# Performance work log

Hardware: AMD Instinct MI355X
Metric: run time of the kernel (lower is better)

## Reference

```python
import jax, jax.numpy as jnp
import numpy as np
import math

B, Q, CQ = 2, 2048, 512
H, D = 8, 64  # no_heads, c_hidden

def setup_inputs() -> dict:
    key = jax.random.key(0)
    ks = jax.random.split(key, 8)
    s = 0.02
    return {
        "q_x": jax.random.normal(ks[0], (B, Q, CQ), jnp.float32),
        "kv_x": jax.random.normal(ks[1], (B, Q, CQ), jnp.float32),
        "bias": jax.random.normal(ks[2], (B, 1, Q, Q), jnp.float32),
        "w_qkv": jax.random.normal(ks[3], (3 * H * D, CQ), jnp.float32) * s,
        "w_o": jax.random.normal(ks[4], (CQ, H * D), jnp.float32) * s,
        "b_o": jnp.zeros((CQ,), jnp.float32),
        "w_g": jax.random.normal(ks[5], (H * D, CQ), jnp.float32) * s,
        "b_g": jnp.zeros((H * D,), jnp.float32),
    }

def reference(q_x, kv_x, bias, w_qkv, w_o, b_o, w_g, b_g):
    # Fused QKV projection from q_x (kv_x is unused by the original module's _prep_qkv)
    qkv = jnp.einsum('bqc,ec->bqe', q_x, w_qkv)  # [B,Q,3*H*D]
    q, k, v = jnp.split(qkv, 3, axis=-1)
    q = q.reshape(B, Q, H, D) / math.sqrt(D)
    k = k.reshape(B, Q, H, D)
    v = v.reshape(B, Q, H, D)
    # scores + additive pairwise bias, softmax over keys
    scores = jnp.einsum('bqhd,bkhd->bhqk', q, k) + bias  # [B,H,Q,K]
    attn = jax.nn.softmax(scores, axis=-1)
    o = jnp.einsum('bhqk,bkhd->bqhd', attn, v)  # [B,Q,H,D]
    # sigmoid gating
    g = jax.nn.sigmoid(jnp.einsum('bqc,ec->bqe', q_x, w_g) + b_g).reshape(B, Q, H, D)
    o = o * g
    # output projection
    o = o.reshape(B, Q, H * D)
    return jnp.einsum('bqe,ce->bqc', o, w_o) + b_o
```

## Files before the change

### kernel.cpp

```cpp
#include <hip/hip_runtime.h>
#include <math.h>

#define B_  2
#define Q_  2048
#define CQ_ 512
#define H_  8
#define D_  64
#define M_  (B_*Q_)
#define L2E 1.44269504088896f

typedef __bf16 bf16;
typedef __bf16 bf16x4 __attribute__((ext_vector_type(4)));
typedef __bf16 bf16x8 __attribute__((ext_vector_type(8)));
typedef float  f32x4  __attribute__((ext_vector_type(4)));
typedef float  f32x16 __attribute__((ext_vector_type(16)));
typedef unsigned int u32x2 __attribute__((ext_vector_type(2)));

__device__ __forceinline__ void gl_lds16(const bf16* g, bf16* l) {
    __builtin_amdgcn_global_load_lds(
        (const __attribute__((address_space(1))) unsigned int*)g,
        (__attribute__((address_space(3))) unsigned int*)l, 16, 0, 0);
}

__device__ __forceinline__ unsigned int cvtpk_bf16(float lo, float hi) {
    unsigned int r;
    asm("v_cvt_pk_bf16_f32 %0, %1, %2" : "=v"(r) : "v"(lo), "v"(hi));
    return r;
}

#define S0 (4096*512)
#define S1 (1536*512)
#define S2 (512*512)
#define S3 (512*512)
__global__ __launch_bounds__(256)
void convert_kernel(const float* __restrict__ qx, const float* __restrict__ wqkv,
                    const float* __restrict__ wg, const float* __restrict__ wo,
                    bf16* __restrict__ qxb, bf16* __restrict__ wcat, bf16* __restrict__ wob)
{
    const long long t = (long long)blockIdx.x * 256 + threadIdx.x;
    const long long e = t * 8;
    const float* src; bf16* dst;
    if (e < S0)                { src = qx + e;                  dst = qxb + e; }
    else if (e < S0 + S1)      { src = wqkv + (e - S0);         dst = wcat + (e - S0); }
    else if (e < S0 + S1 + S2) { src = wg + (e - S0 - S1);      dst = wcat + S1 + (e - S0 - S1); }
    else                       { src = wo + (e - S0 - S1 - S2); dst = wob + (e - S0 - S1 - S2); }
    const float4 a = *(const float4*)(src);
    const float4 b = *(const float4*)(src + 4);
    bf16x8 v;
    v[0] = (bf16)a.x; v[1] = (bf16)a.y; v[2] = (bf16)a.z; v[3] = (bf16)a.w;
    v[4] = (bf16)b.x; v[5] = (bf16)b.y; v[6] = (bf16)b.z; v[7] = (bf16)b.w;
    *(bf16x8*)dst = v;
}

__global__ __launch_bounds__(256)
void bias_rearrange(const float* __restrict__ bias, float* __restrict__ bT)
{
    __shared__ float lds[2048];
    const int x = blockIdx.x;
    const int b = x >> 11, q32 = (x >> 5) & 63, kt = x & 31;
    const int t = threadIdx.x;
    const int qo = t >> 3, kc = (t & 7) * 8;
    const float* src = bias + ((size_t)b * Q_ + q32 * 32 + qo) * Q_ + kt * 64 + kc;
    const float4 a = *(const float4*)src;
    const float4 c = *(const float4*)(src + 4);
    const float v[8] = {a.x, a.y, a.z, a.w, c.x, c.y, c.z, c.w};
    #pragma unroll
    for (int j2 = 0; j2 < 8; ++j2) {
        const int ko = kc + j2;
        const int i  = (ko >> 5) * 4 + ((ko >> 3) & 3);
        const int b5 = (ko >> 2) & 1;
        const int j  = ko & 3;
        lds[i * 256 + b5 * 128 + qo * 4 + j] = v[j2];
    }
    __syncthreads();
    float* outp = bT + ((size_t)(b * 64 + q32) * 32 + kt) * 2048 + t * 8;
    *(float4*)(outp)     = *(const float4*)(lds + t * 8);
    *(float4*)(outp + 4) = *(const float4*)(lds + t * 8 + 4);
}

template<int BM, int BN, int EPI>
__global__ __launch_bounds__(256)
void gemm_bf16(const bf16* __restrict__ A, const bf16* __restrict__ W,
               const float* __restrict__ bvec, float* __restrict__ fout,
               bf16* __restrict__ qb, bf16* __restrict__ kb, bf16* __restrict__ vb,
               bf16* __restrict__ gb)
{
    constexpr int MI = BM / 32, NJ = BN / 32;
    __shared__ __align__(16) bf16 As[BM * 32];
    __shared__ __align__(16) bf16 Bs[BN * 32];

    const int t = threadIdx.x;
    const int w = t >> 6, lane = t & 63;
    const int l15 = lane & 15, quad = lane >> 4;
    const int wm = w & 1, wn = w >> 1;
    const int bm = blockIdx.x * BM;
    const int bn = blockIdx.y * BN;
    const bool swapped = (EPI == 1) || ((bn >> 9) != 2);

    f32x4 acc[MI][NJ] = {};

    const int rr = t >> 2;
    const int cc = (t & 3) * 8;

    for (int k0 = 0; k0 < 512; k0 += 32) {
        #pragma unroll
        for (int i = 0; i < BM / 64; ++i)
            gl_lds16(A + (size_t)(bm + i * 64 + rr) * 512 + k0 + cc,
                     As + (i * 64 + w * 16) * 32);
        #pragma unroll
        for (int i = 0; i < BN / 64; ++i)
            gl_lds16(W + (size_t)(bn + i * 64 + rr) * 512 + k0 + cc,
                     Bs + (i * 64 + w * 16) * 32);
        __asm__ volatile("s_waitcnt vmcnt(0)" ::: "memory");
        __syncthreads();

        bf16x8 af[MI], bfr[NJ];
        #pragma unroll
        for (int i = 0; i < MI; ++i)
            af[i] = *(const bf16x8*)(As + (wm * (BM / 2) + i * 16 + l15) * 32 + quad * 8);
        #pragma unroll
        for (int j = 0; j < NJ; ++j)
            bfr[j] = *(const bf16x8*)(Bs + (wn * (BN / 2) + j * 16 + l15) * 32 + quad * 8);
        if (swapped) {
            #pragma unroll
            for (int i = 0; i < MI; ++i)
                #pragma unroll
                for (int j = 0; j < NJ; ++j)
                    acc[i][j] = __builtin_amdgcn_mfma_f32_16x16x32_bf16(bfr[j], af[i], acc[i][j], 0, 0, 0);
        } else {
            #pragma unroll
            for (int i = 0; i < MI; ++i)
                #pragma unroll
                for (int j = 0; j < NJ; ++j)
                    acc[i][j] = __builtin_amdgcn_mfma_f32_16x16x32_bf16(af[i], bfr[j], acc[i][j], 0, 0, 0);
        }
        __syncthreads();
    }

    if (swapped) {
        #pragma unroll
        for (int i = 0; i < MI; ++i) {
            const int m = bm + wm * (BM / 2) + i * 16 + l15;
            const int b = m >> 11, qq = m & 2047;
            #pragma unroll
            for (int j = 0; j < NJ; ++j) {
                const int n0 = bn + wn * (BN / 2) + j * 16 + quad * 4;
                const f32x4 cv = acc[i][j];
                if constexpr (EPI == 1) {
                    float4 st;
                    st.x = cv[0] + bvec[n0 + 0];
                    st.y = cv[1] + bvec[n0 + 1];
                    st.z = cv[2] + bvec[n0 + 2];
                    st.w = cv[3] + bvec[n0 + 3];
                    *(float4*)(fout + (size_t)m * 512 + n0) = st;
                } else {
                    const int part = n0 >> 9;
                    if (part == 0) {
                        const int h = (n0 >> 6) & 7, d0 = n0 & 63;
                        bf16x4 q4;
                        #pragma unroll
                        for (int r = 0; r < 4; ++r) q4[r] = (bf16)(cv[r] * (0.125f * L2E));
                        *(bf16x4*)(qb + (size_t)(b * H_ + h) * (Q_ * D_) + (size_t)qq * 64 + d0) = q4;
                    } else if (part == 1) {
                        const int h = (n0 >> 6) & 7, d0 = n0 & 63;
                        const size_t off = (size_t)(b * H_ + h) * (Q_ * D_)
                            + (qq >> 6) * 4096 + ((qq >> 5) & 1) * 2048
                            + (d0 >> 4) * 512 + ((d0 >> 3) & 1) * 256
                            + (qq & 31) * 8 + (d0 & 7);
                        bf16x4 k4;
                        #pragma unroll
                        for (int r = 0; r < 4; ++r) k4[r] = (bf16)cv[r];
                        *(bf16x4*)(kb + off) = k4;
                    } else {
                        const int gcol = n0 & 511;
                        const float4 bv4 = *(const float4*)(bvec + gcol);
                        bf16x4 g4;
                        g4[0] = (bf16)(1.f / (1.f + __expf(-(cv[0] + bv4.x))));
                        g4[1] = (bf16)(1.f / (1.f + __expf(-(cv[1] + bv4.y))));
                        g4[2] = (bf16)(1.f / (1.f + __expf(-(cv[2] + bv4.z))));
                        g4[3] = (bf16)(1.f / (1.f + __expf(-(cv[3] + bv4.w))));
                        *(bf16x4*)(gb + (size_t)m * 512 + gcol) = g4;
                    }
                }
            }
        }
    } else {
        #pragma unroll
        for (int i = 0; i < MI; ++i) {
            const int m0 = bm + wm * (BM / 2) + i * 16 + quad * 4;
            const int b = m0 >> 11, qq0 = m0 & 2047;
            #pragma unroll
            for (int j = 0; j < NJ; ++j) {
                const int n = bn + wn * (BN / 2) + j * 16 + l15;
                const int h = (n >> 6) & 7, d = n & 63;
                const size_t off = (size_t)(b * H_ + h) * (Q_ * D_)
                    + (qq0 >> 6) * 4096 + (d >> 5) * 2048
                    + ((qq0 & 63) >> 4) * 512 + ((qq0 >> 3) & 1) * 256
                    + (d & 31) * 8 + (qq0 & 7);
                bf16x4 v4;
                #pragma unroll
                for (int r = 0; r < 4; ++r) v4[r] = (bf16)acc[i][j][r];
                *(bf16x4*)(vb + off) = v4;
            }
        }
    }
}

__global__ __launch_bounds__(256, 3)
void attn_part(const bf16* __restrict__ qb, const bf16* __restrict__ kf,
               const bf16* __restrict__ vf, const float* __restrict__ bT,
               bf16* __restrict__ po, float2* __restrict__ ml)
{
    __shared__ __align__(16) bf16 Ks[2][4096];
    __shared__ __align__(16) bf16 Vs[2][4096];

    const int tid  = threadIdx.x;
    const int wv   = tid >> 6, lane = tid & 63;
    const int l31  = lane & 31, b5 = lane >> 5;
    const int x    = blockIdx.x;
    const int bh   = ((x & 7) << 1) | (x >> 3);
    const int b    = bh >> 3;
    const int qg   = blockIdx.y * 128 + wv * 32 + l31;
    const int ks   = blockIdx.z;
    const int t0   = ks * 11;
    const int nt   = (ks < 2) ? 11 : 10;

    const bf16* qp = qb + ((size_t)bh * Q_ + qg) * D_;
    bf16x8 bq[4];
    #pragma unroll
    for (int c = 0; c < 4; ++c)
        bq[c] = *(const bf16x8*)(qp + c * 16 + b5 * 8);

    f32x16 acc[2] = {};
    float m_run = -INFINITY, l_run = 0.f;

    const bf16*  kfb  = kf + (size_t)bh * (Q_ * D_) + (size_t)t0 * 4096;
    const bf16*  vfb  = vf + (size_t)bh * (Q_ * D_) + (size_t)t0 * 4096;
    const int q32 = blockIdx.y * 4 + wv;
    const float* brow = bT + (((size_t)b * 64 + q32) * 32 + t0) * 2048;

    f32x4 nb[8];

    #pragma unroll
    for (int p = 0; p < 2; ++p) {
        gl_lds16(kfb + (wv * 2 + p) * 512 + lane * 8, Ks[0] + (wv * 2 + p) * 512);
        gl_lds16(vfb + (wv * 2 + p) * 512 + lane * 8, Vs[0] + (wv * 2 + p) * 512);
    }
    #pragma unroll
    for (int i = 0; i < 8; ++i)
        nb[i] = *(const f32x4*)(brow + i * 256 + lane * 4);
    __asm__ volatile("s_waitcnt vmcnt(0)" ::: "memory");
    __syncthreads();

    int cur = 0;
    #pragma unroll 1
    for (int t = 0; t < nt; ++t) {
        if (t < nt - 1) {
            const size_t off = (size_t)(t + 1) * 4096;
            #pragma unroll
            for (int p = 0; p < 2; ++p) {
                gl_lds16(kfb + off + (wv * 2 + p) * 512 + lane * 8,
                         Ks[cur ^ 1] + (wv * 2 + p) * 512);
                gl_lds16(vfb + off + (wv * 2 + p) * 512 + lane * 8,
                         Vs[cur ^ 1] + (wv * 2 + p) * 512);
            }
        }
        __asm__ volatile("" ::: "memory");

        f32x16 sv[2];
        #pragma unroll
        for (int kg = 0; kg < 2; ++kg)
            #pragma unroll
            for (int r = 0; r < 16; ++r)
                sv[kg][r] = nb[kg * 4 + (r >> 2)][r & 3] * L2E;

        if (t < nt - 1) {
            const float* bnx = brow + (size_t)(t + 1) * 2048;
            #pragma unroll
            for (int i = 0; i < 8; ++i)
                nb[i] = *(const f32x4*)(bnx + i * 256 + lane * 4);
        }
        __asm__ volatile("" ::: "memory");

        const bf16* Kc = Ks[cur];
        __builtin_amdgcn_s_setprio(1);
        #pragma unroll
        for (int kg = 0; kg < 2; ++kg)
            #pragma unroll
            for (int c = 0; c < 4; ++c) {
                const bf16x8 ak = *(const bf16x8*)(Kc + kg * 2048 + c * 512 + lane * 8);
                sv[kg] = __builtin_amdgcn_mfma_f32_32x32x16_bf16(ak, bq[c], sv[kg], 0, 0, 0);
            }
        __builtin_amdgcn_s_setprio(0);

        float mx[16];
        #pragma unroll
        for (int r = 0; r < 16; ++r) mx[r] = fmaxf(sv[0][r], sv[1][r]);
        #pragma unroll
        for (int r = 0; r < 8; ++r) mx[r] = fmaxf(mx[r], mx[r + 8]);
        #pragma unroll
        for (int r = 0; r < 4; ++r) mx[r] = fmaxf(mx[r], mx[r + 4]);
        float tmax = fmaxf(fmaxf(mx[0], mx[1]), fmaxf(mx[2], mx[3]));
        tmax = fmaxf(tmax, __shfl_xor(tmax, 32, 64));

        const float mn = fmaxf(m_run, tmax);
        const float alpha = __builtin_amdgcn_exp2f(m_run - mn);
        m_run = mn;

        #pragma unroll
        for (int kg = 0; kg < 2; ++kg)
            #pragma unroll
            for (int r = 0; r < 16; ++r)
                sv[kg][r] = __builtin_amdgcn_exp2f(sv[kg][r] - mn);

        float sm[16];
        #pragma unroll
        for (int r = 0; r < 16; ++r) sm[r] = sv[0][r] + sv[1][r];
        #pragma unroll
        for (int r = 0; r < 8; ++r) sm[r] += sm[r + 8];
        #pragma unroll
        for (int r = 0; r < 4; ++r) sm[r] += sm[r + 4];
        float rsum = (sm[0] + sm[1]) + (sm[2] + sm[3]);
        rsum += __shfl_xor(rsum, 32, 64);
        l_run = l_run * alpha + rsum;
        acc[0] *= alpha;
        acc[1] *= alpha;

        bf16x8 bp[4];
        #pragma unroll
        for (int kg = 0; kg < 2; ++kg)
            #pragma unroll
            for (int h = 0; h < 2; ++h) {
                const unsigned int u  = cvtpk_bf16(sv[kg][8 * h + 0], sv[kg][8 * h + 1]);
                const unsigned int u2 = cvtpk_bf16(sv[kg][8 * h + 2], sv[kg][8 * h + 3]);
                const unsigned int vv = cvtpk_bf16(sv[kg][8 * h + 4], sv[kg][8 * h + 5]);
                const unsigned int v2 = cvtpk_bf16(sv[kg][8 * h + 6], sv[kg][8 * h + 7]);
                const u32x2 s1 = __builtin_amdgcn_permlane32_swap(u,  vv, false, false);
                const u32x2 s2 = __builtin_amdgcn_permlane32_swap(u2, v2, false, false);
                union { unsigned int w[4]; bf16x8 v8; } pkw;
                pkw.w[0] = s1[0]; pkw.w[1] = s2[0]; pkw.w[2] = s1[1]; pkw.w[3] = s2[1];
                bp[kg * 2 + h] = pkw.v8;
            }

        const bf16* Vc = Vs[cur];
        __builtin_amdgcn_s_setprio(1);
        #pragma unroll
        for (int c4 = 0; c4 < 4; ++c4) {
            #pragma unroll
            for (int dg = 0; dg < 2; ++dg) {
                const bf16x8 av = *(const bf16x8*)(Vc + dg * 2048 + c4 * 512 + lane * 8);
                acc[dg] = __builtin_amdgcn_mfma_f32_32x32x16_bf16(av, bp[c4], acc[dg], 0, 0, 0);
            }
        }
        __builtin_amdgcn_s_setprio(0);

        __asm__ volatile("s_waitcnt vmcnt(8)" ::: "memory");
        __syncthreads();
        cur ^= 1;
    }

    const float inv = 1.f / l_run;
    const size_t pbase = ((size_t)(ks * 16 + bh) * Q_ + qg) * 64;
    #pragma unroll
    for (int dg = 0; dg < 2; ++dg)
        #pragma unroll
        for (int gi = 0; gi < 4; ++gi) {
            const int d0 = dg * 32 + gi * 8 + b5 * 4;
            bf16x4 ov;
            #pragma unroll
            for (int r = 0; r < 4; ++r)
                ov[r] = (bf16)(acc[dg][gi * 4 + r] * inv);
            *(bf16x4*)(po + pbase + d0) = ov;
        }
    if (b5 == 0)
        ml[(size_t)(ks * 16 + bh) * Q_ + qg] = make_float2(m_run, l_run);
}

__global__ __launch_bounds__(256)
void merge_kernel(const bf16* __restrict__ po, const float2* __restrict__ ml,
                  const bf16* __restrict__ g, bf16* __restrict__ og)
{
    const int gid = blockIdx.x * 256 + threadIdx.x;
    const int row = gid >> 3;
    const int d8  = (gid & 7) * 8;
    const int bh  = row >> 11, qg = row & 2047;
    const int b   = bh >> 3, h = bh & 7;

    float2 m4[3];
    #pragma unroll
    for (int s = 0; s < 3; ++s) m4[s] = ml[(size_t)s * (16 * Q_) + row];
    const float M = fmaxf(fmaxf(m4[0].x, m4[1].x), m4[2].x);
    float w[3], tot = 0.f;
    #pragma unroll
    for (int s = 0; s < 3; ++s) {
        w[s] = m4[s].y * __builtin_amdgcn_exp2f(m4[s].x - M);
        tot += w[s];
    }
    const float inv = 1.f / tot;
    #pragma unroll
    for (int s = 0; s < 3; ++s) w[s] *= inv;

    bf16x8 o[3];
    #pragma unroll
    for (int s = 0; s < 3; ++s)
        o[s] = *(const bf16x8*)(po + (size_t)s * (16 * Q_ * 64) + (size_t)row * 64 + d8);

    const size_t obase = ((size_t)(b * Q_ + qg)) * 512 + h * 64 + d8;
    const bf16x8 gv = *(const bf16x8*)(g + obase);
    bf16x8 ov;
    #pragma unroll
    for (int r = 0; r < 8; ++r) {
        float acc = 0.f;
        #pragma unroll
        for (int s = 0; s < 3; ++s) acc += (float)o[s][r] * w[s];
        ov[r] = (bf16)(acc * (float)gv[r]);
    }
    *(bf16x8*)(og + obase) = ov;
}

extern "C" void kernel_launch(void* const* d_in, const int* in_sizes, int n_in,
                              void* d_out, int out_size, void* d_ws, size_t ws_size,
                              hipStream_t stream)
{
    const float* q_x   = (const float*)d_in[0];
    const float* bias  = (const float*)d_in[2];
    const float* w_qkv = (const float*)d_in[3];
    const float* w_o   = (const float*)d_in[4];
    const float* b_o   = (const float*)d_in[5];
    const float* w_g   = (const float*)d_in[6];
    const float* b_g   = (const float*)d_in[7];
    float* out = (float*)d_out;

    char* ws = (char*)d_ws;
    bf16*   qxb  = (bf16*)(ws);
    bf16*   wcat = (bf16*)(ws + (4u  << 20));
    bf16*   po   = (bf16*)(ws);
    bf16*   qb   = (bf16*)(ws + (16u << 20));
    bf16*   kb   = (bf16*)(ws + (20u << 20));
    bf16*   vb   = (bf16*)(ws + (24u << 20));
    bf16*   gb   = (bf16*)(ws + (28u << 20));
    bf16*   ogb  = (bf16*)(ws + (32u << 20));
    bf16*   wob  = (bf16*)(ws + (36u << 20));
    float2* ml   = (float2*)(ws + (36u << 20) + (1u << 19));
    float*  bT   = (float*)(ws + (38u << 20));

    convert_kernel<<<(S0 + S1 + S2 + S3) / (256 * 8), 256, 0, stream>>>(
        q_x, w_qkv, w_g, w_o, qxb, wcat, wob);
    bias_rearrange<<<B_ * 64 * 32, 256, 0, stream>>>(bias, bT);
    gemm_bf16<128, 128, 0><<<dim3(32, 16), 256, 0, stream>>>(
        qxb, wcat, b_g, nullptr, qb, kb, vb, gb);
    attn_part<<<dim3(B_ * H_, Q_ / 128, 3), 256, 0, stream>>>(qb, kb, vb, bT, po, ml);
    merge_kernel<<<(16 * Q_ * 8) / 256, 256, 0, stream>>>(po, ml, gb, ogb);
    gemm_bf16<64, 128, 1><<<dim3(64, 4), 256, 0, stream>>>(
        ogb, wob, b_o, out, nullptr, nullptr, nullptr, nullptr);
}
```

Before: 178.8 us.

## Fuse prep kernels, fold split-K merge into output GEMM, lazy softmax rescale

Merges the bf16 conversion and bias rearrangement into one launch and pre-multiplies the bias by log2(e) there, removing a per-tile multiply in attention. The attention loop now skips the running-max update and accumulator rescale when the new tile max stays within 8 (log2 units) of the current max, across the whole wavefront. The split-K merge and gating are moved into the A-tile load of a dedicated output GEMM, which removes a kernel launch and the intermediate gated-output buffer round trip. In exchange, each of the 4 column blocks of the output GEMM recomputes the merge, and the lazy rescale relies on exp2 of values up to 2^8 staying in range.

```diff
diff --git a/kernel.cpp b/kernel.cpp
--- a/kernel.cpp
+++ b/kernel.cpp
@@ -32,56 +32,57 @@
 #define S1 (1536*512)
 #define S2 (512*512)
 #define S3 (512*512)
+#define NCV ((S0 + S1 + S2 + S3) / (256 * 8))
 __global__ __launch_bounds__(256)
 void convert_kernel(const float* __restrict__ qx, const float* __restrict__ wqkv,
                     const float* __restrict__ wg, const float* __restrict__ wo,
-                    bf16* __restrict__ qxb, bf16* __restrict__ wcat, bf16* __restrict__ wob)
-{
-    const long long t = (long long)blockIdx.x * 256 + threadIdx.x;
-    const long long e = t * 8;
-    const float* src; bf16* dst;
-    if (e < S0)                { src = qx + e;                  dst = qxb + e; }
-    else if (e < S0 + S1)      { src = wqkv + (e - S0);         dst = wcat + (e - S0); }
-    else if (e < S0 + S1 + S2) { src = wg + (e - S0 - S1);      dst = wcat + S1 + (e - S0 - S1); }
-    else                       { src = wo + (e - S0 - S1 - S2); dst = wob + (e - S0 - S1 - S2); }
-    const float4 a = *(const float4*)(src);
-    const float4 b = *(const float4*)(src + 4);
-    bf16x8 v;
-    v[0] = (bf16)a.x; v[1] = (bf16)a.y; v[2] = (bf16)a.z; v[3] = (bf16)a.w;
-    v[4] = (bf16)b.x; v[5] = (bf16)b.y; v[6] = (bf16)b.z; v[7] = (bf16)b.w;
-    *(bf16x8*)dst = v;
-}
-
-__global__ __launch_bounds__(256)
-void bias_rearrange(const float* __restrict__ bias, float* __restrict__ bT)
+                    const float* __restrict__ bias,
+                    bf16* __restrict__ qxb, bf16* __restrict__ wcat,
+                    bf16* __restrict__ wob, float* __restrict__ bT)
 {
     __shared__ float lds[2048];
-    const int x = blockIdx.x;
-    const int b = x >> 11, q32 = (x >> 5) & 63, kt = x & 31;
-    const int t = threadIdx.x;
-    const int qo = t >> 3, kc = (t & 7) * 8;
-    const float* src = bias + ((size_t)b * Q_ + q32 * 32 + qo) * Q_ + kt * 64 + kc;
-    const float4 a = *(const float4*)src;
-    const float4 c = *(const float4*)(src + 4);
-    const float v[8] = {a.x, a.y, a.z, a.w, c.x, c.y, c.z, c.w};
-    #pragma unroll
-    for (int j2 = 0; j2 < 8; ++j2) {
-        const int ko = kc + j2;
-        const int i  = (ko >> 5) * 4 + ((ko >> 3) & 3);
-        const int b5 = (ko >> 2) & 1;
-        const int j  = ko & 3;
-        lds[i * 256 + b5 * 128 + qo * 4 + j] = v[j2];
-    }
-    __syncthreads();
-    float* outp = bT + ((size_t)(b * 64 + q32) * 32 + kt) * 2048 + t * 8;
-    *(float4*)(outp)     = *(const float4*)(lds + t * 8);
-    *(float4*)(outp + 4) = *(const float4*)(lds + t * 8 + 4);
-}
-
-template<int BM, int BN, int EPI>
+    const int bx = blockIdx.x;
+    const int t  = threadIdx.x;
+    if (bx < NCV) {
+        const long long e = ((long long)bx * 256 + t) * 8;
+        const float* src; bf16* dst;
+        if (e < S0)                { src = qx + e;                  dst = qxb + e; }
+        else if (e < S0 + S1)      { src = wqkv + (e - S0);         dst = wcat + (e - S0); }
+        else if (e < S0 + S1 + S2) { src = wg + (e - S0 - S1);      dst = wcat + S1 + (e - S0 - S1); }
+        else                       { src = wo + (e - S0 - S1 - S2); dst = wob + (e - S0 - S1 - S2); }
+        const float4 a = *(const float4*)(src);
+        const float4 b = *(const float4*)(src + 4);
+        bf16x8 v;
+        v[0] = (bf16)a.x; v[1] = (bf16)a.y; v[2] = (bf16)a.z; v[3] = (bf16)a.w;
+        v[4] = (bf16)b.x; v[5] = (bf16)b.y; v[6] = (bf16)b.z; v[7] = (bf16)b.w;
+        *(bf16x8*)dst = v;
+    } else {
+        const int x = bx - NCV;
+        const int b = x >> 11, q32 = (x >> 5) & 63, kt = x & 31;
+        const int qo = t >> 3, kc = (t & 7) * 8;
+        const float* src = bias + ((size_t)b * Q_ + q32 * 32 + qo) * Q_ + kt * 64 + kc;
+        const float4 a = *(const float4*)src;
+        const float4 c = *(const float4*)(src + 4);
+        const float v[8] = {a.x, a.y, a.z, a.w, c.x, c.y, c.z, c.w};
+        #pragma unroll
+        for (int j2 = 0; j2 < 8; ++j2) {
+            const int ko = kc + j2;
+            const int i  = (ko >> 5) * 4 + ((ko >> 3) & 3);
+            const int b5 = (ko >> 2) & 1;
+            const int j  = ko & 3;
+            lds[i * 256 + b5 * 128 + qo * 4 + j] = v[j2] * L2E;
+        }
+        __syncthreads();
+        float* outp = bT + ((size_t)(b * 64 + q32) * 32 + kt) * 2048 + t * 8;
+        *(float4*)(outp)     = *(const float4*)(lds + t * 8);
+        *(float4*)(outp + 4) = *(const float4*)(lds + t * 8 + 4);
+    }
+}
+
+template<int BM, int BN>
 __global__ __launch_bounds__(256)
 void gemm_bf16(const bf16* __restrict__ A, const bf16* __restrict__ W,
-               const float* __restrict__ bvec, float* __restrict__ fout,
+               const float* __restrict__ bvec,
                bf16* __restrict__ qb, bf16* __restrict__ kb, bf16* __restrict__ vb,
                bf16* __restrict__ gb)
 {
@@ -95,7 +96,7 @@
     const int wm = w & 1, wn = w >> 1;
     const int bm = blockIdx.x * BM;
     const int bn = blockIdx.y * BN;
-    const bool swapped = (EPI == 1) || ((bn >> 9) != 2);
+    const bool swapped = ((bn >> 9) != 2);
 
     f32x4 acc[MI][NJ] = {};
 
@@ -146,41 +147,32 @@
             for (int j = 0; j < NJ; ++j) {
                 const int n0 = bn + wn * (BN / 2) + j * 16 + quad * 4;
                 const f32x4 cv = acc[i][j];
-                if constexpr (EPI == 1) {
-                    float4 st;
-                    st.x = cv[0] + bvec[n0 + 0];
-                    st.y = cv[1] + bvec[n0 + 1];
-                    st.z = cv[2] + bvec[n0 + 2];
-                    st.w = cv[3] + bvec[n0 + 3];
-                    *(float4*)(fout + (size_t)m * 512 + n0) = st;
+                const int part = n0 >> 9;
+                if (part == 0) {
+                    const int h = (n0 >> 6) & 7, d0 = n0 & 63;
+                    bf16x4 q4;
+                    #pragma unroll
+                    for (int r = 0; r < 4; ++r) q4[r] = (bf16)(cv[r] * (0.125f * L2E));
+                    *(bf16x4*)(qb + (size_t)(b * H_ + h) * (Q_ * D_) + (size_t)qq * 64 + d0) = q4;
+                } else if (part == 1) {
+                    const int h = (n0 >> 6) & 7, d0 = n0 & 63;
+                    const size_t off = (size_t)(b * H_ + h) * (Q_ * D_)
+                        + (qq >> 6) * 4096 + ((qq >> 5) & 1) * 2048
+                        + (d0 >> 4) * 512 + ((d0 >> 3) & 1) * 256
+                        + (qq & 31) * 8 + (d0 & 7);
+                    bf16x4 k4;
+                    #pragma unroll
+                    for (int r = 0; r < 4; ++r) k4[r] = (bf16)cv[r];
+                    *(bf16x4*)(kb + off) = k4;
                 } else {
-                    const int part = n0 >> 9;
-                    if (part == 0) {
-                        const int h = (n0 >> 6) & 7, d0 = n0 & 63;
-                        bf16x4 q4;
-                        #pragma unroll
-                        for (int r = 0; r < 4; ++r) q4[r] = (bf16)(cv[r] * (0.125f * L2E));
-                        *(bf16x4*)(qb + (size_t)(b * H_ + h) * (Q_ * D_) + (size_t)qq * 64 + d0) = q4;
-                    } else if (part == 1) {
-                        const int h = (n0 >> 6) & 7, d0 = n0 & 63;
-                        const size_t off = (size_t)(b * H_ + h) * (Q_ * D_)
-                            + (qq >> 6) * 4096 + ((qq >> 5) & 1) * 2048
-                            + (d0 >> 4) * 512 + ((d0 >> 3) & 1) * 256
-                            + (qq & 31) * 8 + (d0 & 7);
-                        bf16x4 k4;
-                        #pragma unroll
-                        for (int r = 0; r < 4; ++r) k4[r] = (bf16)cv[r];
-                        *(bf16x4*)(kb + off) = k4;
-                    } else {
-                        const int gcol = n0 & 511;
-                        const float4 bv4 = *(const float4*)(bvec + gcol);
-                        bf16x4 g4;
-                        g4[0] = (bf16)(1.f / (1.f + __expf(-(cv[0] + bv4.x))));
-                        g4[1] = (bf16)(1.f / (1.f + __expf(-(cv[1] + bv4.y))));
-                        g4[2] = (bf16)(1.f / (1.f + __expf(-(cv[2] + bv4.z))));
-                        g4[3] = (bf16)(1.f / (1.f + __expf(-(cv[3] + bv4.w))));
-                        *(bf16x4*)(gb + (size_t)m * 512 + gcol) = g4;
-                    }
+                    const int gcol = n0 & 511;
+                    const float4 bv4 = *(const float4*)(bvec + gcol);
+                    bf16x4 g4;
+                    g4[0] = (bf16)(1.f / (1.f + __expf(-(cv[0] + bv4.x))));
+                    g4[1] = (bf16)(1.f / (1.f + __expf(-(cv[1] + bv4.y))));
+                    g4[2] = (bf16)(1.f / (1.f + __expf(-(cv[2] + bv4.z))));
+                    g4[3] = (bf16)(1.f / (1.f + __expf(-(cv[3] + bv4.w))));
+                    *(bf16x4*)(gb + (size_t)m * 512 + gcol) = g4;
                 }
             }
         }
@@ -272,7 +264,7 @@
         for (int kg = 0; kg < 2; ++kg)
             #pragma unroll
             for (int r = 0; r < 16; ++r)
-                sv[kg][r] = nb[kg * 4 + (r >> 2)][r & 3] * L2E;
+                sv[kg][r] = nb[kg * 4 + (r >> 2)][r & 3];
 
         if (t < nt - 1) {
             const float* bnx = brow + (size_t)(t + 1) * 2048;
@@ -303,8 +295,9 @@
         float tmax = fmaxf(fmaxf(mx[0], mx[1]), fmaxf(mx[2], mx[3]));
         tmax = fmaxf(tmax, __shfl_xor(tmax, 32, 64));
 
-        const float mn = fmaxf(m_run, tmax);
-        const float alpha = __builtin_amdgcn_exp2f(m_run - mn);
+        const float m_old = m_run;
+        const bool keep = (__all(tmax <= m_old + 8.f) != 0);
+        const float mn = keep ? m_old : fmaxf(m_old, tmax);
         m_run = mn;
 
         #pragma unroll
@@ -322,9 +315,14 @@
         for (int r = 0; r < 4; ++r) sm[r] += sm[r + 4];
         float rsum = (sm[0] + sm[1]) + (sm[2] + sm[3]);
         rsum += __shfl_xor(rsum, 32, 64);
-        l_run = l_run * alpha + rsum;
-        acc[0] *= alpha;
-        acc[1] *= alpha;
+        if (keep) {
+            l_run += rsum;
+        } else {
+            const float alpha = __builtin_amdgcn_exp2f(m_old - mn);
+            l_run = l_run * alpha + rsum;
+            acc[0] *= alpha;
+            acc[1] *= alpha;
+        }
 
         bf16x8 bp[4];
         #pragma unroll
@@ -377,45 +375,92 @@
 }
 
 __global__ __launch_bounds__(256)
-void merge_kernel(const bf16* __restrict__ po, const float2* __restrict__ ml,
-                  const bf16* __restrict__ g, bf16* __restrict__ og)
+void gemm_out(const bf16* __restrict__ po, const float2* __restrict__ ml,
+              const bf16* __restrict__ gb, const bf16* __restrict__ W,
+              const float* __restrict__ bvec, float* __restrict__ fout)
 {
-    const int gid = blockIdx.x * 256 + threadIdx.x;
-    const int row = gid >> 3;
-    const int d8  = (gid & 7) * 8;
-    const int bh  = row >> 11, qg = row & 2047;
-    const int b   = bh >> 3, h = bh & 7;
-
-    float2 m4[3];
+    constexpr int BM = 64, BN = 128, MI = BM / 32, NJ = BN / 32;
+    __shared__ __align__(16) bf16 As[BM * 32];
+    __shared__ __align__(16) bf16 Bs[BN * 32];
+
+    const int t = threadIdx.x;
+    const int w = t >> 6, lane = t & 63;
+    const int l15 = lane & 15, quad = lane >> 4;
+    const int wm = w & 1, wn = w >> 1;
+    const int bm = blockIdx.x * BM;
+    const int bn = blockIdx.y * BN;
+
+    const int rr = t >> 2;
+    const int cc = (t & 3) * 8;
+    const int m  = bm + rr;
+    const int b  = m >> 11, qq = m & 2047;
+
+    f32x4 acc[MI][NJ] = {};
+
+    for (int k0 = 0; k0 < 512; k0 += 32) {
+        #pragma unroll
+        for (int i = 0; i < BN / 64; ++i)
+            gl_lds16(W + (size_t)(bn + i * 64 + rr) * 512 + k0 + cc,
+                     Bs + (i * 64 + w * 16) * 32);
+
+        {
+            const int c0 = k0 + cc;
+            const int h  = c0 >> 6, d8 = c0 & 63;
+            const int prow = (b * 8 + h) * 2048 + qq;
+            const float2 m0 = ml[prow];
+            const float2 m1 = ml[32768 + prow];
+            const float2 m2 = ml[65536 + prow];
+            const float Mx = fmaxf(fmaxf(m0.x, m1.x), m2.x);
+            float w0 = m0.y * __builtin_amdgcn_exp2f(m0.x - Mx);
+            float w1 = m1.y * __builtin_amdgcn_exp2f(m1.x - Mx);
+            float w2 = m2.y * __builtin_amdgcn_exp2f(m2.x - Mx);
+            const float inv = 1.f / (w0 + w1 + w2);
+            w0 *= inv; w1 *= inv; w2 *= inv;
+            const bf16x8 p0 = *(const bf16x8*)(po + (size_t)prow * 64 + d8);
+            const bf16x8 p1 = *(const bf16x8*)(po + (size_t)(32768 + prow) * 64 + d8);
+            const bf16x8 p2 = *(const bf16x8*)(po + (size_t)(65536 + prow) * 64 + d8);
+            const bf16x8 gv = *(const bf16x8*)(gb + (size_t)m * 512 + c0);
+            bf16x8 av;
+            #pragma unroll
+            for (int r = 0; r < 8; ++r)
+                av[r] = (bf16)(((float)p0[r] * w0 + (float)p1[r] * w1 +
+                                (float)p2[r] * w2) * (float)gv[r]);
+            *(bf16x8*)(As + t * 8) = av;
+        }
+
+        __asm__ volatile("s_waitcnt vmcnt(0)" ::: "memory");
+        __syncthreads();
+
+        bf16x8 af[MI], bfr[NJ];
+        #pragma unroll
+        for (int i = 0; i < MI; ++i)
+            af[i] = *(const bf16x8*)(As + (wm * (BM / 2) + i * 16 + l15) * 32 + quad * 8);
+        #pragma unroll
+        for (int j = 0; j < NJ; ++j)
+            bfr[j] = *(const bf16x8*)(Bs + (wn * (BN / 2) + j * 16 + l15) * 32 + quad * 8);
+        #pragma unroll
+        for (int i = 0; i < MI; ++i)
+            #pragma unroll
+            for (int j = 0; j < NJ; ++j)
+                acc[i][j] = __builtin_amdgcn_mfma_f32_16x16x32_bf16(bfr[j], af[i], acc[i][j], 0, 0, 0);
+        __syncthreads();
+    }
+
     #pragma unroll
-    for (int s = 0; s < 3; ++s) m4[s] = ml[(size_t)s * (16 * Q_) + row];
-    const float M = fmaxf(fmaxf(m4[0].x, m4[1].x), m4[2].x);
-    float w[3], tot = 0.f;
-    #pragma unroll
-    for (int s = 0; s < 3; ++s) {
-        w[s] = m4[s].y * __builtin_amdgcn_exp2f(m4[s].x - M);
-        tot += w[s];
-    }
-    const float inv = 1.f / tot;
-    #pragma unroll
-    for (int s = 0; s < 3; ++s) w[s] *= inv;
-
-    bf16x8 o[3];
-    #pragma unroll
-    for (int s = 0; s < 3; ++s)
-        o[s] = *(const bf16x8*)(po + (size_t)s * (16 * Q_ * 64) + (size_t)row * 64 + d8);
-
-    const size_t obase = ((size_t)(b * Q_ + qg)) * 512 + h * 64 + d8;
-    const bf16x8 gv = *(const bf16x8*)(g + obase);
-    bf16x8 ov;
-    #pragma unroll
-    for (int r = 0; r < 8; ++r) {
-        float acc = 0.f;
-        #pragma unroll
-        for (int s = 0; s < 3; ++s) acc += (float)o[s][r] * w[s];
-        ov[r] = (bf16)(acc * (float)gv[r]);
-    }
-    *(bf16x8*)(og + obase) = ov;
+    for (int i = 0; i < MI; ++i) {
+        const int mm = bm + wm * (BM / 2) + i * 16 + l15;
+        #pragma unroll
+        for (int j = 0; j < NJ; ++j) {
+            const int n0 = bn + wn * (BN / 2) + j * 16 + quad * 4;
+            const f32x4 cv = acc[i][j];
+            float4 st;
+            st.x = cv[0] + bvec[n0 + 0];
+            st.y = cv[1] + bvec[n0 + 1];
+            st.z = cv[2] + bvec[n0 + 2];
+            st.w = cv[3] + bvec[n0 + 3];
+            *(float4*)(fout + (size_t)mm * 512 + n0) = st;
+        }
+    }
 }
 
 extern "C" void kernel_launch(void* const* d_in, const int* in_sizes, int n_in,
@@ -439,18 +484,14 @@
     bf16*   kb   = (bf16*)(ws + (20u << 20));
     bf16*   vb   = (bf16*)(ws + (24u << 20));
     bf16*   gb   = (bf16*)(ws + (28u << 20));
-    bf16*   ogb  = (bf16*)(ws + (32u << 20));
     bf16*   wob  = (bf16*)(ws + (36u << 20));
     float2* ml   = (float2*)(ws + (36u << 20) + (1u << 19));
     float*  bT   = (float*)(ws + (38u << 20));
 
-    convert_kernel<<<(S0 + S1 + S2 + S3) / (256 * 8), 256, 0, stream>>>(
-        q_x, w_qkv, w_g, w_o, qxb, wcat, wob);
-    bias_rearrange<<<B_ * 64 * 32, 256, 0, stream>>>(bias, bT);
-    gemm_bf16<128, 128, 0><<<dim3(32, 16), 256, 0, stream>>>(
-        qxb, wcat, b_g, nullptr, qb, kb, vb, gb);
+    convert_kernel<<<NCV + B_ * 64 * 32, 256, 0, stream>>>(
+        q_x, w_qkv, w_g, w_o, bias, qxb, wcat, wob, bT);
+    gemm_bf16<128, 128><<<dim3(32, 16), 256, 0, stream>>>(
+        qxb, wcat, b_g, qb, kb, vb, gb);
     attn_part<<<dim3(B_ * H_, Q_ / 128, 3), 256, 0, stream>>>(qb, kb, vb, bT, po, ml);
-    merge_kernel<<<(16 * Q_ * 8) / 256, 256, 0, stream>>>(po, ml, gb, ogb);
-    gemm_bf16<64, 128, 1><<<dim3(64, 4), 256, 0, stream>>>(
-        ogb, wob, b_o, out, nullptr, nullptr, nullptr, nullptr);
-}
+    gemm_out<<<dim3(64, 4), 256, 0, stream>>>(po, ml, gb, wob, b_o, out);
+}
```

Result: no change. 178.4 us (-0.2%).
